# Optimization experiments

Hardware: AMD Instinct MI355X
Metric: run time of the kernel (lower is better)

## Reference

```python
import jax, jax.numpy as jnp
import numpy as np
from jax import lax

N_CHANNELS = 64
N_FILTERS = 256
N_LAYERS = 9  # residual blocks use dilations 2**1 .. 2**(N_LAYERS-1)


def causal_conv1d(x, w, dilation):
    """Causal dilated conv. x: [B,T,Cin], w: [K,Cin,Cout]."""
    pad = (w.shape[0] - 1) * dilation
    return lax.conv_general_dilated(
        x, w, window_strides=(1,), padding=[(pad, 0)],
        rhs_dilation=(dilation,), dimension_numbers=("NWC", "WIO", "NWC"))


def setup_inputs() -> dict:
    key = jax.random.key(0)
    ks = jax.random.split(key, 12)
    B, T, C, F, L = 8, 4096, N_CHANNELS, N_FILTERS, N_LAYERS
    s = lambda fan_in: 1.0 / np.sqrt(fan_in)
    return {
        "x": jax.random.normal(ks[0], (B, T, C), jnp.float32),
        "Wc": jax.random.normal(ks[1], (2, C, F), jnp.float32) * s(2 * C),
        "Wf": jax.random.normal(ks[2], (L - 1, 2, F, F), jnp.float32) * s(2 * F),
        "Wg": jax.random.normal(ks[3], (L - 1, 2, F, F), jnp.float32) * s(2 * F),
        "Wr": jax.random.normal(ks[4], (L - 1, F, F), jnp.float32) * s(F),
        "br": jnp.zeros((L - 1, F), jnp.float32),
        "Ws": jax.random.normal(ks[5], (L - 1, F, F), jnp.float32) * s(F),
        "bs": jnp.zeros((L - 1, F), jnp.float32),
        "Wd1": jax.random.normal(ks[6], (F, C), jnp.float32) * s(F),
        "bd1": jnp.zeros((C,), jnp.float32),
        "Wd2": jax.random.normal(ks[7], (C, C), jnp.float32) * s(C),
        "bd2": jnp.zeros((C,), jnp.float32),
    }


def reference(x, Wc, Wf, Wg, Wr, br, Ws, bs, Wd1, bd1, Wd2, bd2):
    # Initial causal conv, dilation 1, no bias.
    out = causal_conv1d(x, Wc, 1)  # [B,T,F]
    skip_sum = jnp.zeros_like(out)
    for i in range(N_LAYERS - 1):
        d = 2 ** (i + 1)
        f = causal_conv1d(out, Wf[i], d)
        g = causal_conv1d(out, Wg[i], d)
        z = jnp.tanh(f) * jax.nn.sigmoid(g)
        out = out + jnp.einsum("btf,fo->bto", z, Wr[i]) + br[i]
        skip_sum = skip_sum + jnp.einsum("btf,fo->bto", z, Ws[i]) + bs[i]
    h = jax.nn.selu(skip_sum)
    h = jnp.einsum("btf,fc->btc", h, Wd1) + bd1
    h = jax.nn.selu(h)
    h = jnp.einsum("btc,co->bto", h, Wd2) + bd2
    return h
```

## Files before the change

kernel.cpp:

```cpp
#include <hip/hip_runtime.h>
#include <cstdint>

typedef unsigned short u16;
typedef unsigned int u32;
typedef __attribute__((ext_vector_type(8))) short s8v;
typedef __attribute__((ext_vector_type(4))) float f4v;

#define FCH 256

__device__ __forceinline__ float bf2f(u16 u){ return __uint_as_float(((u32)u)<<16); }
__device__ __forceinline__ u16 f2bf(float x){
  u32 u = __float_as_uint(x);
  u += 0x7fffu + ((u>>16)&1u);
  return (u16)(u>>16);
}
__device__ __forceinline__ uint4 pack8(float4 a, float4 b){
  uint4 o;
  o.x = (u32)f2bf(a.x) | ((u32)f2bf(a.y)<<16);
  o.y = (u32)f2bf(a.z) | ((u32)f2bf(a.w)<<16);
  o.z = (u32)f2bf(b.x) | ((u32)f2bf(b.y)<<16);
  o.w = (u32)f2bf(b.z) | ((u32)f2bf(b.w)<<16);
  return o;
}
__device__ __forceinline__ float seluf(float x){
  const float sc = 1.0507009873554805f, al = 1.6732632423543772f;
  return x > 0.f ? sc*x : sc*al*(__expf(x)-1.f);
}

__global__ __launch_bounds__(256) void pack_kernel(
    const float* __restrict__ Wc, const float* __restrict__ Wf, const float* __restrict__ Wg,
    const float* __restrict__ Wr, const float* __restrict__ Ws,
    const float* __restrict__ Wd1, const float* __restrict__ Wd2,
    u16* __restrict__ Bp1, u16* __restrict__ Bp2, u16* __restrict__ Bp0,
    u16* __restrict__ BpD1, u16* __restrict__ BpD2)
{
  int gid = blockIdx.x*256 + threadIdx.x;
  int frag = gid >> 6;
  int lane = gid & 63;
  int q = lane >> 4, i15 = lane & 15;
  u16 v[8];
  u16* dst;
  if (frag < 4096) {
    int layer = frag >> 9, rem = frag & 511;
    int kc = rem >> 5, nt = rem & 31;
    int n = nt*16 + i15;
    const float* W = (n < 256) ? Wf : Wg;
    int nn = (n < 256) ? n : n - 256;
    #pragma unroll
    for (int j = 0; j < 8; ++j) {
      int k = kc*32 + q*8 + j;
      int tap = k >> 8, cin = k & 255;
      v[j] = f2bf(W[((size_t)((layer*2 + tap)*256 + cin))*256 + nn]);
    }
    dst = Bp1 + (size_t)frag*512 + lane*8;
  } else if (frag < 6144) {
    int f = frag - 4096;
    int layer = f >> 8, rem = f & 255;
    int kc = rem >> 5, nt = rem & 31;
    int n = nt*16 + i15;
    const float* W = (n < 256) ? Wr : Ws;
    int nn = (n < 256) ? n : n - 256;
    #pragma unroll
    for (int j = 0; j < 8; ++j) {
      int k = kc*32 + q*8 + j;
      v[j] = f2bf(W[((size_t)(layer*256 + k))*256 + nn]);
    }
    dst = Bp2 + (size_t)f*512 + lane*8;
  } else if (frag < 6208) {
    int f = frag - 6144;
    int kc = f >> 4, nt = f & 15;
    int n = nt*16 + i15;
    #pragma unroll
    for (int j = 0; j < 8; ++j) {
      int k = kc*32 + q*8 + j;
      int tap = k >> 6, cin = k & 63;
      v[j] = f2bf(Wc[(size_t)(tap*64 + cin)*256 + n]);
    }
    dst = Bp0 + (size_t)f*512 + lane*8;
  } else if (frag < 6240) {
    int f = frag - 6208;
    int kc = f >> 2, nt = f & 3;
    int n = nt*16 + i15;
    #pragma unroll
    for (int j = 0; j < 8; ++j) {
      int k = kc*32 + q*8 + j;
      v[j] = f2bf(Wd1[(size_t)k*64 + n]);
    }
    dst = BpD1 + (size_t)f*512 + lane*8;
  } else if (frag < 6248) {
    int f = frag - 6240;
    int kc = f >> 2, nt = f & 3;
    int n = nt*16 + i15;
    #pragma unroll
    for (int j = 0; j < 8; ++j) {
      int k = kc*32 + q*8 + j;
      v[j] = f2bf(Wd2[(size_t)k*64 + n]);
    }
    dst = BpD2 + (size_t)f*512 + lane*8;
  } else return;
  uint4 o;
  o.x = (u32)v[0] | ((u32)v[1] << 16);
  o.y = (u32)v[2] | ((u32)v[3] << 16);
  o.z = (u32)v[4] | ((u32)v[5] << 16);
  o.w = (u32)v[6] | ((u32)v[7] << 16);
  *reinterpret_cast<uint4*>(dst) = o;
}

__global__ __launch_bounds__(256, 2) void conv0_kernel(
    const float* __restrict__ x, u16* __restrict__ outBf,
    const u16* __restrict__ Bp0)
{
  __shared__ __align__(16) u16 ldsA[2][2048];
  const int tid = threadIdx.x;
  const int w = tid >> 6, lane = tid & 63, q = lane >> 4, i15 = lane & 15;
  const int rb = blockIdx.x * 64;
  const int sm = tid >> 2, sg = tid & 3;
  const int grow = rb + sm;
  const int tpos = grow & 4095;
  const int sunit = ((sm >> 4)*64 + sg*16 + ((sm & 15) ^ (sg << 1))) * 8;
  const int runit = (q*16 + (i15 ^ (q << 1))) * 8;

  f4v acc[4][4];
  #pragma unroll
  for (int jj = 0; jj < 4; ++jj)
    #pragma unroll
    for (int mt = 0; mt < 4; ++mt)
      acc[jj][mt] = (f4v){0.f,0.f,0.f,0.f};

  float4 f0 = {0.f,0.f,0.f,0.f}, f1 = {0.f,0.f,0.f,0.f};
  if (tpos >= 1) {
    const float* px = x + (size_t)(grow-1)*64 + sg*8;
    f0 = *reinterpret_cast<const float4*>(px);
    f1 = *reinterpret_cast<const float4*>(px + 4);
  }
  *reinterpret_cast<uint4*>(&ldsA[0][sunit]) = pack8(f0, f1);
  s8v bcur[4], bnxt[4];
  #pragma unroll
  for (int jj = 0; jj < 4; ++jj)
    bcur[jj] = *reinterpret_cast<const s8v*>(Bp0 + ((size_t)(w + 4*jj)*64 + lane)*8);
  __syncthreads();

  for (int kc = 0; kc < 4; ++kc) {
    const int cur = kc & 1;
    uint4 an = {0u,0u,0u,0u};
    if (kc < 3) {
      int kg = (kc+1)*32 + sg*8;
      int tap = kg >> 6, col = kg & 63;
      float4 g0 = {0.f,0.f,0.f,0.f}, g1 = {0.f,0.f,0.f,0.f};
      if (tap) {
        const float* px = x + (size_t)grow*64 + col;
        g0 = *reinterpret_cast<const float4*>(px);
        g1 = *reinterpret_cast<const float4*>(px + 4);
      } else if (tpos >= 1) {
        const float* px = x + (size_t)(grow-1)*64 + col;
        g0 = *reinterpret_cast<const float4*>(px);
        g1 = *reinterpret_cast<const float4*>(px + 4);
      }
      an = pack8(g0, g1);
      #pragma unroll
      for (int jj = 0; jj < 4; ++jj)
        bnxt[jj] = *reinterpret_cast<const s8v*>(Bp0 + (((size_t)(kc+1)*16 + (w + 4*jj))*64 + lane)*8);
    }
    s8v af[4];
    #pragma unroll
    for (int mt = 0; mt < 4; ++mt)
      af[mt] = *reinterpret_cast<const s8v*>(&ldsA[cur][mt*512 + runit]);
    #pragma unroll
    for (int jj = 0; jj < 4; ++jj)
      #pragma unroll
      for (int mt = 0; mt < 4; ++mt)
        acc[jj][mt] = __builtin_amdgcn_mfma_f32_16x16x32_bf16(af[mt], bcur[jj], acc[jj][mt], 0,0,0);
    if (kc < 3) {
      *reinterpret_cast<uint4*>(&ldsA[cur ^ 1][sunit]) = an;
      #pragma unroll
      for (int jj = 0; jj < 4; ++jj) bcur[jj] = bnxt[jj];
    }
    __syncthreads();
  }

  #pragma unroll
  for (int jj = 0; jj < 4; ++jj) {
    const int cc = (w + 4*jj)*16 + i15;
    #pragma unroll
    for (int mt = 0; mt < 4; ++mt)
      #pragma unroll
      for (int r = 0; r < 4; ++r) {
        const int g2 = rb + mt*16 + q*4 + r;
        outBf[(size_t)g2*FCH + cc] = f2bf(acc[jj][mt][r]);
      }
  }
}

__global__ __launch_bounds__(256, 3) void layer_kernel(
    const u16* __restrict__ inBf, u16* __restrict__ outBf,
    u16* __restrict__ skipB,
    const u16* __restrict__ Bp1, const u16* __restrict__ Bp2,
    const float* __restrict__ br, const float* __restrict__ bs,
    int dil, int first)
{
  __shared__ __align__(16) u16 ldsA[2][32*40];
  __shared__ __align__(16) u16 ldsZ[32*264];
  const int tid = threadIdx.x;
  const int w = tid >> 6, lane = tid & 63, q = lane >> 4, i15 = lane & 15;
  const int rb = blockIdx.x * 32;
  const int sm = tid >> 3, sg = tid & 7;
  const int grow = rb + sm;
  const int tpos = grow & 4095;

  f4v acc[8][2];
  #pragma unroll
  for (int jj = 0; jj < 8; ++jj)
    #pragma unroll
    for (int mt = 0; mt < 2; ++mt)
      acc[jj][mt] = (f4v){0.f,0.f,0.f,0.f};

  {
    uint2 a0 = {0u,0u};
    if (tpos >= dil)
      a0 = *reinterpret_cast<const uint2*>(inBf + (size_t)(grow - dil)*FCH + sg*4);
    *reinterpret_cast<uint2*>(&ldsA[0][sm*40 + sg*4]) = a0;
    s8v bcur[8], bnxt[8];
    #pragma unroll
    for (int jj = 0; jj < 8; ++jj)
      bcur[jj] = *reinterpret_cast<const s8v*>(Bp1 + ((size_t)(w + 4*jj)*64 + lane)*8);
    __syncthreads();

    for (int kc = 0; kc < 16; ++kc) {
      const int cur = kc & 1;
      uint2 an = {0u,0u};
      if (kc < 15) {
        int kg = (kc+1)*32 + sg*4;
        int tap = kg >> 8, col = kg & 255;
        if (tap) an = *reinterpret_cast<const uint2*>(inBf + (size_t)grow*FCH + col);
        else if (tpos >= dil) an = *reinterpret_cast<const uint2*>(inBf + (size_t)(grow - dil)*FCH + col);
        #pragma unroll
        for (int jj = 0; jj < 8; ++jj)
          bnxt[jj] = *reinterpret_cast<const s8v*>(Bp1 + (((size_t)(kc+1)*32 + (w + 4*jj))*64 + lane)*8);
      }
      s8v af[2];
      #pragma unroll
      for (int mt = 0; mt < 2; ++mt)
        af[mt] = *reinterpret_cast<const s8v*>(&ldsA[cur][(mt*16 + i15)*40 + q*8]);
      #pragma unroll
      for (int jj = 0; jj < 8; ++jj)
        #pragma unroll
        for (int mt = 0; mt < 2; ++mt)
          acc[jj][mt] = __builtin_amdgcn_mfma_f32_16x16x32_bf16(af[mt], bcur[jj], acc[jj][mt], 0,0,0);
      if (kc < 15) {
        *reinterpret_cast<uint2*>(&ldsA[cur ^ 1][sm*40 + sg*4]) = an;
        #pragma unroll
        for (int jj = 0; jj < 8; ++jj) bcur[jj] = bnxt[jj];
      }
      __syncthreads();
    }
  }

  #pragma unroll
  for (int jj = 0; jj < 4; ++jj) {
    const int colb = (w + 4*jj)*16 + i15;
    #pragma unroll
    for (int mt = 0; mt < 2; ++mt)
      #pragma unroll
      for (int r = 0; r < 4; ++r) {
        float f = acc[jj][mt][r];
        float g = acc[jj+4][mt][r];
        float z = (1.f - 2.f/(__expf(2.f*f) + 1.f)) * (1.f/(1.f + __expf(-g)));
        ldsZ[(mt*16 + q*4 + r)*264 + colb] = f2bf(z);
      }
  }
  __syncthreads();

  #pragma unroll
  for (int jj = 0; jj < 8; ++jj) {
    const int nt = w + 4*jj;
    const bool isR = (jj < 4);
    const int cc = (isR ? nt*16 : (nt-16)*16) + i15;
    const float bias = isR ? br[cc] : bs[cc];
    #pragma unroll
    for (int mt = 0; mt < 2; ++mt)
      #pragma unroll
      for (int r = 0; r < 4; ++r) {
        const int g2 = rb + mt*16 + q*4 + r;
        float vv;
        if (isR) vv = bf2f(inBf[(size_t)g2*FCH + cc]) + bias;
        else     vv = first ? bias : (bf2f(skipB[(size_t)g2*FCH + cc]) + bias);
        acc[jj][mt][r] = vv;
      }
  }

  {
    s8v b2c[8], b2n[8];
    #pragma unroll
    for (int jj = 0; jj < 8; ++jj)
      b2c[jj] = *reinterpret_cast<const s8v*>(Bp2 + ((size_t)(w + 4*jj)*64 + lane)*8);
    for (int kc = 0; kc < 8; ++kc) {
      if (kc < 7) {
        #pragma unroll
        for (int jj = 0; jj < 8; ++jj)
          b2n[jj] = *reinterpret_cast<const s8v*>(Bp2 + (((size_t)(kc+1)*32 + (w + 4*jj))*64 + lane)*8);
      }
      s8v af[2];
      #pragma unroll
      for (int mt = 0; mt < 2; ++mt)
        af[mt] = *reinterpret_cast<const s8v*>(&ldsZ[(mt*16 + i15)*264 + kc*32 + q*8]);
      #pragma unroll
      for (int jj = 0; jj < 8; ++jj)
        #pragma unroll
        for (int mt = 0; mt < 2; ++mt)
          acc[jj][mt] = __builtin_amdgcn_mfma_f32_16x16x32_bf16(af[mt], b2c[jj], acc[jj][mt], 0,0,0);
      if (kc < 7) {
        #pragma unroll
        for (int jj = 0; jj < 8; ++jj) b2c[jj] = b2n[jj];
      }
    }
  }

  #pragma unroll
  for (int jj = 0; jj < 8; ++jj) {
    const int nt = w + 4*jj;
    const bool isR = (jj < 4);
    const int cc = (isR ? nt*16 : (nt-16)*16) + i15;
    #pragma unroll
    for (int mt = 0; mt < 2; ++mt)
      #pragma unroll
      for (int r = 0; r < 4; ++r) {
        const int g2 = rb + mt*16 + q*4 + r;
        u16 hv = f2bf(acc[jj][mt][r]);
        if (isR) outBf[(size_t)g2*FCH + cc] = hv;
        else     skipB[(size_t)g2*FCH + cc] = hv;
      }
  }
}

__global__ __launch_bounds__(256, 2) void final_kernel(
    const u16* __restrict__ skipB, const u16* __restrict__ BpD1, const u16* __restrict__ BpD2,
    const float* __restrict__ bd1, const float* __restrict__ bd2, float* __restrict__ outp)
{
  __shared__ __align__(16) u16 ldsH[64*264];
  __shared__ __align__(16) u16 ldsH2[64*72];
  const int tid = threadIdx.x;
  const int w = tid >> 6, lane = tid & 63, q = lane >> 4, i15 = lane & 15;
  const int rb = blockIdx.x * 64;
  const int sm = tid >> 2, sseg = tid & 3;

  {
    const u16* sp = skipB + (size_t)(rb + sm)*256 + sseg*64;
    u16* dr = &ldsH[sm*264 + sseg*64];
    #pragma unroll
    for (int u = 0; u < 8; ++u) {
      uint4 raw = *reinterpret_cast<const uint4*>(sp + u*8);
      u32 rr[4] = {raw.x, raw.y, raw.z, raw.w};
      uint4 o;
      u32 oo[4];
      #pragma unroll
      for (int p = 0; p < 4; ++p) {
        float e0 = seluf(bf2f((u16)(rr[p] & 0xffffu)));
        float e1 = seluf(bf2f((u16)(rr[p] >> 16)));
        oo[p] = (u32)f2bf(e0) | ((u32)f2bf(e1) << 16);
      }
      o.x = oo[0]; o.y = oo[1]; o.z = oo[2]; o.w = oo[3];
      *reinterpret_cast<uint4*>(dr + u*8) = o;
    }
  }
  __syncthreads();

  f4v a1[4];
  #pragma unroll
  for (int mt = 0; mt < 4; ++mt) a1[mt] = (f4v){0.f,0.f,0.f,0.f};
  for (int kc = 0; kc < 8; ++kc) {
    s8v b = *reinterpret_cast<const s8v*>(BpD1 + ((size_t)(kc*4 + w)*64 + lane)*8);
    #pragma unroll
    for (int mt = 0; mt < 4; ++mt) {
      s8v af = *reinterpret_cast<const s8v*>(&ldsH[(mt*16 + i15)*264 + kc*32 + q*8]);
      a1[mt] = __builtin_amdgcn_mfma_f32_16x16x32_bf16(af, b, a1[mt], 0,0,0);
    }
  }
  const float bb1 = bd1[w*16 + i15];
  #pragma unroll
  for (int mt = 0; mt < 4; ++mt)
    #pragma unroll
    for (int r = 0; r < 4; ++r)
      ldsH2[(mt*16 + q*4 + r)*72 + w*16 + i15] = f2bf(seluf(a1[mt][r] + bb1));
  __syncthreads();

  f4v a2[4];
  #pragma unroll
  for (int mt = 0; mt < 4; ++mt) a2[mt] = (f4v){0.f,0.f,0.f,0.f};
  #pragma unroll
  for (int kc = 0; kc < 2; ++kc) {
    s8v b = *reinterpret_cast<const s8v*>(BpD2 + ((size_t)(kc*4 + w)*64 + lane)*8);
    #pragma unroll
    for (int mt = 0; mt < 4; ++mt) {
      s8v af = *reinterpret_cast<const s8v*>(&ldsH2[(mt*16 + i15)*72 + kc*32 + q*8]);
      a2[mt] = __builtin_amdgcn_mfma_f32_16x16x32_bf16(af, b, a2[mt], 0,0,0);
    }
  }
  const float bb2 = bd2[w*16 + i15];
  #pragma unroll
  for (int mt = 0; mt < 4; ++mt)
    #pragma unroll
    for (int r = 0; r < 4; ++r)
      outp[(size_t)(rb + mt*16 + q*4 + r)*64 + w*16 + i15] = a2[mt][r] + bb2;
}

__global__ __launch_bounds__(256) void zero_kernel(uint4* __restrict__ outp, int n16)
{
  int i = blockIdx.x*256 + threadIdx.x;
  if (i < n16) outp[i] = (uint4){0u,0u,0u,0u};
}

extern "C" void kernel_launch(void* const* d_in, const int* in_sizes, int n_in,
                              void* d_out, int out_size, void* d_ws, size_t ws_size,
                              hipStream_t stream)
{
  (void)n_in;
  const float* x   = (const float*)d_in[0];
  const float* Wc  = (const float*)d_in[1];
  const float* Wf  = (const float*)d_in[2];
  const float* Wg  = (const float*)d_in[3];
  const float* Wr  = (const float*)d_in[4];
  const float* br  = (const float*)d_in[5];
  const float* Ws  = (const float*)d_in[6];
  const float* bs  = (const float*)d_in[7];
  const float* Wd1 = (const float*)d_in[8];
  const float* bd1 = (const float*)d_in[9];
  const float* Wd2 = (const float*)d_in[10];
  const float* bd2 = (const float*)d_in[11];

  const size_t ROWS = (size_t)in_sizes[0] / 64;
  const int gridC = (int)(ROWS / 64);
  const int gridL = (int)(ROWS / 32);

  const size_t packsB = (size_t)6248 * 512 * 2;
  const size_t bfBuf  = ROWS * 256 * 2;
  const size_t needB = packsB + 3*bfBuf;

  if (ws_size < needB) {
    int n16 = (out_size * 4) / 16;
    zero_kernel<<<(n16 + 255)/256, 256, 0, stream>>>((uint4*)d_out, n16);
    return;
  }

  char* ws = (char*)d_ws;
  u16* Bp1    = (u16*)ws;            ws += (size_t)4096*512*2;
  u16* Bp2    = (u16*)ws;            ws += (size_t)2048*512*2;
  u16* Bp0    = (u16*)ws;            ws += (size_t)64*512*2;
  u16* BpD1   = (u16*)ws;            ws += (size_t)32*512*2;
  u16* BpD2   = (u16*)ws;            ws += (size_t)8*512*2;
  u16* skipB  = (u16*)ws;            ws += bfBuf;
  u16* bufA   = (u16*)ws;            ws += bfBuf;
  u16* bufB   = (u16*)ws;            ws += bfBuf;

  pack_kernel<<<1562, 256, 0, stream>>>(Wc, Wf, Wg, Wr, Ws, Wd1, Wd2,
                                        Bp1, Bp2, Bp0, BpD1, BpD2);
  conv0_kernel<<<gridC, 256, 0, stream>>>(x, bufA, Bp0);
  u16* bufs[2] = {bufA, bufB};
  for (int i = 0; i < 8; ++i) {
    layer_kernel<<<gridL, 256, 0, stream>>>(
        bufs[i & 1], bufs[(i + 1) & 1], skipB,
        Bp1 + (size_t)i*262144, Bp2 + (size_t)i*131072,
        br + i*256, bs + i*256, 2 << i, (i == 0) ? 1 : 0);
  }
  final_kernel<<<gridC, 256, 0, stream>>>(skipB, BpD1, BpD2, bd1, bd2, (float*)d_out);
}
```

Baseline: 591.9 us.

## Double layer-kernel row tile to 64 with swizzled full-K LDS staging and XCD tile remap

Each layer block now handles 64 rows instead of 32, so each loaded weight fragment feeds twice as many MFMAs and weight traffic per row is halved. Each conv tap's whole 64x256 activation slab is staged into one XOR-swizzled LDS buffer, replacing the per-K-chunk double buffer, and the same buffer is reused for the gated z tile. Block indices are remapped so neighbouring tiles land on the same XCD. In exchange, accumulator registers double (acc[8][4]), which may lower occupancy relative to the declared 3 blocks per CU, the grid halves, and global loads are no longer overlapped with the MFMA loop.

```diff
diff --git a/kernel.cpp b/kernel.cpp
--- a/kernel.cpp
+++ b/kernel.cpp
@@ -196,76 +196,107 @@
     u16* __restrict__ skipB,
     const u16* __restrict__ Bp1, const u16* __restrict__ Bp2,
     const float* __restrict__ br, const float* __restrict__ bs,
-    int dil, int first)
-{
-  __shared__ __align__(16) u16 ldsA[2][32*40];
-  __shared__ __align__(16) u16 ldsZ[32*264];
+    int dil, int first, int nT8)
+{
+  __shared__ __align__(16) u16 ldsU[64*256];
   const int tid = threadIdx.x;
   const int w = tid >> 6, lane = tid & 63, q = lane >> 4, i15 = lane & 15;
-  const int rb = blockIdx.x * 32;
-  const int sm = tid >> 3, sg = tid & 7;
-  const int grow = rb + sm;
-  const int tpos = grow & 4095;
-
-  f4v acc[8][2];
+  const int bid = blockIdx.x;
+  const int tile = nT8 ? ((bid & 7) * nT8 + (bid >> 3)) : bid;
+  const int rb = tile * 64;
+
+  f4v acc[8][4];
   #pragma unroll
   for (int jj = 0; jj < 8; ++jj)
     #pragma unroll
-    for (int mt = 0; mt < 2; ++mt)
+    for (int mt = 0; mt < 4; ++mt)
       acc[jj][mt] = (f4v){0.f,0.f,0.f,0.f};
 
-  {
-    uint2 a0 = {0u,0u};
-    if (tpos >= dil)
-      a0 = *reinterpret_cast<const uint2*>(inBf + (size_t)(grow - dil)*FCH + sg*4);
-    *reinterpret_cast<uint2*>(&ldsA[0][sm*40 + sg*4]) = a0;
-    s8v bcur[8], bnxt[8];
+  s8v bcur[8], bnxt[8];
+  #pragma unroll
+  for (int jj = 0; jj < 8; ++jj)
+    bcur[jj] = *reinterpret_cast<const s8v*>(Bp1 + ((size_t)(w + 4*jj)*64 + lane)*8);
+
+  #pragma unroll
+  for (int u = 0; u < 8; ++u) {
+    int f = tid + 256*u;
+    int row = f >> 5, unit = f & 31;
+    int g = rb + row;
+    uint4 v = {0u,0u,0u,0u};
+    if ((g & 4095) >= dil)
+      v = *reinterpret_cast<const uint4*>(inBf + (size_t)(g - dil)*FCH + unit*8);
+    *reinterpret_cast<uint4*>(&ldsU[row*256 + (unit ^ (row & 7))*8]) = v;
+  }
+  __syncthreads();
+
+  for (int kc = 0; kc < 8; ++kc) {
     #pragma unroll
     for (int jj = 0; jj < 8; ++jj)
-      bcur[jj] = *reinterpret_cast<const s8v*>(Bp1 + ((size_t)(w + 4*jj)*64 + lane)*8);
-    __syncthreads();
-
-    for (int kc = 0; kc < 16; ++kc) {
-      const int cur = kc & 1;
-      uint2 an = {0u,0u};
-      if (kc < 15) {
-        int kg = (kc+1)*32 + sg*4;
-        int tap = kg >> 8, col = kg & 255;
-        if (tap) an = *reinterpret_cast<const uint2*>(inBf + (size_t)grow*FCH + col);
-        else if (tpos >= dil) an = *reinterpret_cast<const uint2*>(inBf + (size_t)(grow - dil)*FCH + col);
-        #pragma unroll
-        for (int jj = 0; jj < 8; ++jj)
-          bnxt[jj] = *reinterpret_cast<const s8v*>(Bp1 + (((size_t)(kc+1)*32 + (w + 4*jj))*64 + lane)*8);
-      }
-      s8v af[2];
-      #pragma unroll
-      for (int mt = 0; mt < 2; ++mt)
-        af[mt] = *reinterpret_cast<const s8v*>(&ldsA[cur][(mt*16 + i15)*40 + q*8]);
+      bnxt[jj] = *reinterpret_cast<const s8v*>(Bp1 + (((size_t)(kc+1)*32 + (w + 4*jj))*64 + lane)*8);
+    s8v af[4];
+    #pragma unroll
+    for (int mt = 0; mt < 4; ++mt)
+      af[mt] = *reinterpret_cast<const s8v*>(&ldsU[(mt*16 + i15)*256 + ((kc*4 + q) ^ (i15 & 7))*8]);
+    #pragma unroll
+    for (int jj = 0; jj < 8; ++jj)
+      #pragma unroll
+      for (int mt = 0; mt < 4; ++mt)
+        acc[jj][mt] = __builtin_amdgcn_mfma_f32_16x16x32_bf16(af[mt], bcur[jj], acc[jj][mt], 0,0,0);
+    #pragma unroll
+    for (int jj = 0; jj < 8; ++jj) bcur[jj] = bnxt[jj];
+  }
+  __syncthreads();
+
+  #pragma unroll
+  for (int u = 0; u < 8; ++u) {
+    int f = tid + 256*u;
+    int row = f >> 5, unit = f & 31;
+    int g = rb + row;
+    uint4 v = *reinterpret_cast<const uint4*>(inBf + (size_t)g*FCH + unit*8);
+    *reinterpret_cast<uint4*>(&ldsU[row*256 + (unit ^ (row & 7))*8]) = v;
+  }
+  __syncthreads();
+
+  for (int kc = 8; kc < 16; ++kc) {
+    if (kc < 15) {
       #pragma unroll
       for (int jj = 0; jj < 8; ++jj)
-        #pragma unroll
-        for (int mt = 0; mt < 2; ++mt)
-          acc[jj][mt] = __builtin_amdgcn_mfma_f32_16x16x32_bf16(af[mt], bcur[jj], acc[jj][mt], 0,0,0);
-      if (kc < 15) {
-        *reinterpret_cast<uint2*>(&ldsA[cur ^ 1][sm*40 + sg*4]) = an;
-        #pragma unroll
-        for (int jj = 0; jj < 8; ++jj) bcur[jj] = bnxt[jj];
-      }
-      __syncthreads();
-    }
-  }
+        bnxt[jj] = *reinterpret_cast<const s8v*>(Bp1 + (((size_t)(kc+1)*32 + (w + 4*jj))*64 + lane)*8);
+    }
+    s8v af[4];
+    #pragma unroll
+    for (int mt = 0; mt < 4; ++mt)
+      af[mt] = *reinterpret_cast<const s8v*>(&ldsU[(mt*16 + i15)*256 + (((kc & 7)*4 + q) ^ (i15 & 7))*8]);
+    #pragma unroll
+    for (int jj = 0; jj < 8; ++jj)
+      #pragma unroll
+      for (int mt = 0; mt < 4; ++mt)
+        acc[jj][mt] = __builtin_amdgcn_mfma_f32_16x16x32_bf16(af[mt], bcur[jj], acc[jj][mt], 0,0,0);
+    if (kc < 15) {
+      #pragma unroll
+      for (int jj = 0; jj < 8; ++jj) bcur[jj] = bnxt[jj];
+    }
+  }
+  __syncthreads();
+
+  s8v b2c[8], b2n[8];
+  #pragma unroll
+  for (int jj = 0; jj < 8; ++jj)
+    b2c[jj] = *reinterpret_cast<const s8v*>(Bp2 + ((size_t)(w + 4*jj)*64 + lane)*8);
 
   #pragma unroll
   for (int jj = 0; jj < 4; ++jj) {
     const int colb = (w + 4*jj)*16 + i15;
-    #pragma unroll
-    for (int mt = 0; mt < 2; ++mt)
+    const int unit = colb >> 3, rem = colb & 7;
+    #pragma unroll
+    for (int mt = 0; mt < 4; ++mt)
       #pragma unroll
       for (int r = 0; r < 4; ++r) {
         float f = acc[jj][mt][r];
         float g = acc[jj+4][mt][r];
         float z = (1.f - 2.f/(__expf(2.f*f) + 1.f)) * (1.f/(1.f + __expf(-g)));
-        ldsZ[(mt*16 + q*4 + r)*264 + colb] = f2bf(z);
+        int mrow = mt*16 + q*4 + r;
+        ldsU[mrow*256 + (unit ^ (mrow & 7))*8 + rem] = f2bf(z);
       }
   }
   __syncthreads();
@@ -277,7 +308,7 @@
     const int cc = (isR ? nt*16 : (nt-16)*16) + i15;
     const float bias = isR ? br[cc] : bs[cc];
     #pragma unroll
-    for (int mt = 0; mt < 2; ++mt)
+    for (int mt = 0; mt < 4; ++mt)
       #pragma unroll
       for (int r = 0; r < 4; ++r) {
         const int g2 = rb + mt*16 + q*4 + r;
@@ -288,30 +319,24 @@
       }
   }
 
-  {
-    s8v b2c[8], b2n[8];
+  for (int kc = 0; kc < 8; ++kc) {
+    if (kc < 7) {
+      #pragma unroll
+      for (int jj = 0; jj < 8; ++jj)
+        b2n[jj] = *reinterpret_cast<const s8v*>(Bp2 + (((size_t)(kc+1)*32 + (w + 4*jj))*64 + lane)*8);
+    }
+    s8v af[4];
+    #pragma unroll
+    for (int mt = 0; mt < 4; ++mt)
+      af[mt] = *reinterpret_cast<const s8v*>(&ldsU[(mt*16 + i15)*256 + ((kc*4 + q) ^ (i15 & 7))*8]);
     #pragma unroll
     for (int jj = 0; jj < 8; ++jj)
-      b2c[jj] = *reinterpret_cast<const s8v*>(Bp2 + ((size_t)(w + 4*jj)*64 + lane)*8);
-    for (int kc = 0; kc < 8; ++kc) {
-      if (kc < 7) {
-        #pragma unroll
-        for (int jj = 0; jj < 8; ++jj)
-          b2n[jj] = *reinterpret_cast<const s8v*>(Bp2 + (((size_t)(kc+1)*32 + (w + 4*jj))*64 + lane)*8);
-      }
-      s8v af[2];
-      #pragma unroll
-      for (int mt = 0; mt < 2; ++mt)
-        af[mt] = *reinterpret_cast<const s8v*>(&ldsZ[(mt*16 + i15)*264 + kc*32 + q*8]);
-      #pragma unroll
-      for (int jj = 0; jj < 8; ++jj)
-        #pragma unroll
-        for (int mt = 0; mt < 2; ++mt)
-          acc[jj][mt] = __builtin_amdgcn_mfma_f32_16x16x32_bf16(af[mt], b2c[jj], acc[jj][mt], 0,0,0);
-      if (kc < 7) {
-        #pragma unroll
-        for (int jj = 0; jj < 8; ++jj) b2c[jj] = b2n[jj];
-      }
+      #pragma unroll
+      for (int mt = 0; mt < 4; ++mt)
+        acc[jj][mt] = __builtin_amdgcn_mfma_f32_16x16x32_bf16(af[mt], b2c[jj], acc[jj][mt], 0,0,0);
+    if (kc < 7) {
+      #pragma unroll
+      for (int jj = 0; jj < 8; ++jj) b2c[jj] = b2n[jj];
     }
   }
 
@@ -321,7 +346,7 @@
     const bool isR = (jj < 4);
     const int cc = (isR ? nt*16 : (nt-16)*16) + i15;
     #pragma unroll
-    for (int mt = 0; mt < 2; ++mt)
+    for (int mt = 0; mt < 4; ++mt)
       #pragma unroll
       for (int r = 0; r < 4; ++r) {
         const int g2 = rb + mt*16 + q*4 + r;
@@ -429,7 +454,8 @@
 
   const size_t ROWS = (size_t)in_sizes[0] / 64;
   const int gridC = (int)(ROWS / 64);
-  const int gridL = (int)(ROWS / 32);
+  const int nTiles = gridC;
+  const int nT8 = (nTiles % 8 == 0) ? nTiles / 8 : 0;
 
   const size_t packsB = (size_t)6248 * 512 * 2;
   const size_t bfBuf  = ROWS * 256 * 2;
@@ -456,10 +482,10 @@
   conv0_kernel<<<gridC, 256, 0, stream>>>(x, bufA, Bp0);
   u16* bufs[2] = {bufA, bufB};
   for (int i = 0; i < 8; ++i) {
-    layer_kernel<<<gridL, 256, 0, stream>>>(
+    layer_kernel<<<nTiles, 256, 0, stream>>>(
         bufs[i & 1], bufs[(i + 1) & 1], skipB,
         Bp1 + (size_t)i*262144, Bp2 + (size_t)i*131072,
-        br + i*256, bs + i*256, 2 << i, (i == 0) ? 1 : 0);
+        br + i*256, bs + i*256, 2 << i, (i == 0) ? 1 : 0, nT8);
   }
   final_kernel<<<gridC, 256, 0, stream>>>(skipB, BpD1, BpD2, bd1, bd2, (float*)d_out);
 }
```

New measurement: 1.156 ms. 1.95x slower.

## Load A fragments directly from global into registers, drop LDS staging and barriers

Applied to the files above, without the earlier changes.

The first GEMM of the layer kernel no longer stages the activation tile through double-buffered LDS with a barrier every K-chunk. Each lane now loads its MFMA A-fragment (16 bytes) straight from global memory into a register double buffer, with the causal-tap zero handling kept. Column tiles are remapped so each wave owns contiguous n-tiles, which moves one barrier after the residual/skip init. Every wave now fetches the A rows redundantly from global/L2 instead of sharing them through LDS, and register pressure rises.

```diff
diff --git a/kernel.cpp b/kernel.cpp
--- a/kernel.cpp
+++ b/kernel.cpp
@@ -198,14 +198,10 @@
     const float* __restrict__ br, const float* __restrict__ bs,
     int dil, int first)
 {
-  __shared__ __align__(16) u16 ldsA[2][32*40];
   __shared__ __align__(16) u16 ldsZ[32*264];
   const int tid = threadIdx.x;
   const int w = tid >> 6, lane = tid & 63, q = lane >> 4, i15 = lane & 15;
   const int rb = blockIdx.x * 32;
-  const int sm = tid >> 3, sg = tid & 7;
-  const int grow = rb + sm;
-  const int tpos = grow & 4095;
 
   f4v acc[8][2];
   #pragma unroll
@@ -214,50 +210,60 @@
     for (int mt = 0; mt < 2; ++mt)
       acc[jj][mt] = (f4v){0.f,0.f,0.f,0.f};
 
+  const int gr[2] = { rb + i15, rb + 16 + i15 };
+  const bool ok0[2] = { (gr[0] & 4095) >= dil, (gr[1] & 4095) >= dil };
+  const u16* a0[2] = { inBf + (size_t)(gr[0] - dil)*FCH,
+                       inBf + (size_t)(gr[1] - dil)*FCH };
+  const u16* a1[2] = { inBf + (size_t)gr[0]*FCH,
+                       inBf + (size_t)gr[1]*FCH };
+  const int colq = q*8;
+
   {
-    uint2 a0 = {0u,0u};
-    if (tpos >= dil)
-      a0 = *reinterpret_cast<const uint2*>(inBf + (size_t)(grow - dil)*FCH + sg*4);
-    *reinterpret_cast<uint2*>(&ldsA[0][sm*40 + sg*4]) = a0;
-    s8v bcur[8], bnxt[8];
-    #pragma unroll
-    for (int jj = 0; jj < 8; ++jj)
-      bcur[jj] = *reinterpret_cast<const s8v*>(Bp1 + ((size_t)(w + 4*jj)*64 + lane)*8);
-    __syncthreads();
-
+    s8v bbuf[2][8];
+    uint4 abuf[2][2];
+    #pragma unroll
+    for (int jj = 0; jj < 8; ++jj) {
+      int nt = (jj < 4) ? (w*4 + jj) : (16 + w*4 + (jj - 4));
+      bbuf[0][jj] = *reinterpret_cast<const s8v*>(Bp1 + ((size_t)nt*64 + lane)*8);
+    }
+    #pragma unroll
+    for (int mt = 0; mt < 2; ++mt) {
+      uint4 v = {0u,0u,0u,0u};
+      if (ok0[mt]) v = *reinterpret_cast<const uint4*>(a0[mt] + colq);
+      abuf[0][mt] = v;
+    }
     for (int kc = 0; kc < 16; ++kc) {
       const int cur = kc & 1;
-      uint2 an = {0u,0u};
       if (kc < 15) {
-        int kg = (kc+1)*32 + sg*4;
-        int tap = kg >> 8, col = kg & 255;
-        if (tap) an = *reinterpret_cast<const uint2*>(inBf + (size_t)grow*FCH + col);
-        else if (tpos >= dil) an = *reinterpret_cast<const uint2*>(inBf + (size_t)(grow - dil)*FCH + col);
+        const int kn = kc + 1;
         #pragma unroll
-        for (int jj = 0; jj < 8; ++jj)
-          bnxt[jj] = *reinterpret_cast<const s8v*>(Bp1 + (((size_t)(kc+1)*32 + (w + 4*jj))*64 + lane)*8);
-      }
-      s8v af[2];
-      #pragma unroll
-      for (int mt = 0; mt < 2; ++mt)
-        af[mt] = *reinterpret_cast<const s8v*>(&ldsA[cur][(mt*16 + i15)*40 + q*8]);
+        for (int jj = 0; jj < 8; ++jj) {
+          int nt = (jj < 4) ? (w*4 + jj) : (16 + w*4 + (jj - 4));
+          bbuf[cur ^ 1][jj] = *reinterpret_cast<const s8v*>(
+              Bp1 + (((size_t)kn*32 + nt)*64 + lane)*8);
+        }
+        const int tap = kn >> 3, col = (kn & 7)*32 + colq;
+        #pragma unroll
+        for (int mt = 0; mt < 2; ++mt) {
+          uint4 v = {0u,0u,0u,0u};
+          if (tap) v = *reinterpret_cast<const uint4*>(a1[mt] + col);
+          else if (ok0[mt]) v = *reinterpret_cast<const uint4*>(a0[mt] + col);
+          abuf[cur ^ 1][mt] = v;
+        }
+      }
       #pragma unroll
       for (int jj = 0; jj < 8; ++jj)
         #pragma unroll
         for (int mt = 0; mt < 2; ++mt)
-          acc[jj][mt] = __builtin_amdgcn_mfma_f32_16x16x32_bf16(af[mt], bcur[jj], acc[jj][mt], 0,0,0);
-      if (kc < 15) {
-        *reinterpret_cast<uint2*>(&ldsA[cur ^ 1][sm*40 + sg*4]) = an;
-        #pragma unroll
-        for (int jj = 0; jj < 8; ++jj) bcur[jj] = bnxt[jj];
-      }
-      __syncthreads();
+          acc[jj][mt] = __builtin_amdgcn_mfma_f32_16x16x32_bf16(
+              *reinterpret_cast<const s8v*>(&abuf[cur][mt]), bbuf[cur][jj],
+              acc[jj][mt], 0,0,0);
     }
   }
 
   #pragma unroll
   for (int jj = 0; jj < 4; ++jj) {
-    const int colb = (w + 4*jj)*16 + i15;
+    const int colb = (w*4 + jj)*16 + i15;
     #pragma unroll
     for (int mt = 0; mt < 2; ++mt)
       #pragma unroll
@@ -268,13 +274,11 @@
         ldsZ[(mt*16 + q*4 + r)*264 + colb] = f2bf(z);
       }
   }
-  __syncthreads();
 
   #pragma unroll
   for (int jj = 0; jj < 8; ++jj) {
-    const int nt = w + 4*jj;
     const bool isR = (jj < 4);
-    const int cc = (isR ? nt*16 : (nt-16)*16) + i15;
+    const int cc = (isR ? (w*4 + jj) : (w*4 + jj - 4))*16 + i15;
     const float bias = isR ? br[cc] : bs[cc];
     #pragma unroll
     for (int mt = 0; mt < 2; ++mt)
@@ -287,39 +291,42 @@
         acc[jj][mt][r] = vv;
       }
   }
+  __syncthreads();
 
   {
-    s8v b2c[8], b2n[8];
-    #pragma unroll
-    for (int jj = 0; jj < 8; ++jj)
-      b2c[jj] = *reinterpret_cast<const s8v*>(Bp2 + ((size_t)(w + 4*jj)*64 + lane)*8);
+    s8v bbuf[2][8];
+    #pragma unroll
+    for (int jj = 0; jj < 8; ++jj) {
+      int nt = (jj < 4) ? (w*4 + jj) : (16 + w*4 + (jj - 4));
+      bbuf[0][jj] = *reinterpret_cast<const s8v*>(Bp2 + ((size_t)nt*64 + lane)*8);
+    }
     for (int kc = 0; kc < 8; ++kc) {
+      const int cur = kc & 1;
       if (kc < 7) {
         #pragma unroll
-        for (int jj = 0; jj < 8; ++jj)
-          b2n[jj] = *reinterpret_cast<const s8v*>(Bp2 + (((size_t)(kc+1)*32 + (w + 4*jj))*64 + lane)*8);
+        for (int jj = 0; jj < 8; ++jj) {
+          int nt = (jj < 4) ? (w*4 + jj) : (16 + w*4 + (jj - 4));
+          bbuf[cur ^ 1][jj] = *reinterpret_cast<const s8v*>(
+              Bp2 + (((size_t)(kc+1)*32 + nt)*64 + lane)*8);
+        }
       }
       s8v af[2];
       #pragma unroll
       for (int mt = 0; mt < 2; ++mt)
-        af[mt] = *reinterpret_cast<const s8v*>(&ldsZ[(mt*16 + i15)*264 + kc*32 + q*8]);
+        af[mt] = *reinterpret_cast<const s8v*>(&ldsZ[(mt*16 + i15)*264 + kc*32 + colq]);
       #pragma unroll
       for (int jj = 0; jj < 8; ++jj)
         #pragma unroll
         for (int mt = 0; mt < 2; ++mt)
-          acc[jj][mt] = __builtin_amdgcn_mfma_f32_16x16x32_bf16(af[mt], b2c[jj], acc[jj][mt], 0,0,0);
-      if (kc < 7) {
-        #pragma unroll
-        for (int jj = 0; jj < 8; ++jj) b2c[jj] = b2n[jj];
-      }
+          acc[jj][mt] = __builtin_amdgcn_mfma_f32_16x16x32_bf16(
+              af[mt], bbuf[cur][jj], acc[jj][mt], 0,0,0);
     }
   }
 
   #pragma unroll
   for (int jj = 0; jj < 8; ++jj) {
-    const int nt = w + 4*jj;
     const bool isR = (jj < 4);
-    const int cc = (isR ? nt*16 : (nt-16)*16) + i15;
+    const int cc = (isR ? (w*4 + jj) : (w*4 + jj - 4))*16 + i15;
     #pragma unroll
     for (int mt = 0; mt < 2; ++mt)
       #pragma unroll
```

After: 848.5 us. 1.43x slower.
